# Kernel tuning notes

Measured on AMD Instinct MI355X. Metric: run time of the kernel, lower is better.

## Reference

```python
import jax, jax.numpy as jnp
import numpy as np

N_NODES = 50000
N_EDGES = 800000
D = 128
LN_EPS = 1e-5


def setup_inputs() -> dict:
    key = jax.random.key(0)
    ks = jax.random.split(key, 8)
    s = 1.0 / np.sqrt(D)
    return {
        "x": jax.random.normal(ks[0], (N_NODES, D), jnp.float32),
        "edge_index": jax.random.randint(ks[1], (2, N_EDGES), 0, N_NODES, jnp.int64),
        "W1l": jax.random.normal(ks[2], (D, D), jnp.float32) * s,
        "b1l": jnp.zeros((D,), jnp.float32),
        "W1r": jax.random.normal(ks[3], (D, D), jnp.float32) * s,
        "W2l": jax.random.normal(ks[4], (D, D), jnp.float32) * s,
        "b2l": jnp.zeros((D,), jnp.float32),
        "W2r": jax.random.normal(ks[5], (D, D), jnp.float32) * s,
        "ln_w": jnp.ones((D,), jnp.float32),
        "ln_b": jnp.zeros((D,), jnp.float32),
    }


def _sage_conv(h, edge_index, Wl, bl, Wr):
    # PyG SAGEConv (mean aggr): out = lin_l(mean_{j in N(i)} h_j) + lin_r(h_i)
    src, dst = edge_index[0], edge_index[1]
    n = h.shape[0]
    msg_sum = jax.ops.segment_sum(h[src], dst, num_segments=n)      # [N, D]
    cnt = jax.ops.segment_sum(jnp.ones_like(src, h.dtype), dst, num_segments=n)
    mean = msg_sum / jnp.maximum(cnt, 1.0)[:, None]                  # 0 for isolated
    return mean @ Wl.T + bl + h @ Wr.T


def _layer_norm(h, w, b):
    mu = jnp.mean(h, axis=-1, keepdims=True)
    var = jnp.mean(jnp.square(h - mu), axis=-1, keepdims=True)
    return (h - mu) * jax.lax.rsqrt(var + LN_EPS) * w + b


def reference(x, edge_index, W1l, b1l, W1r, W2l, b2l, W2r, ln_w, ln_b):
    h = jax.nn.relu(_sage_conv(x, edge_index, W1l, b1l, W1r))
    h = jax.nn.relu(_sage_conv(h, edge_index, W2l, b2l, W2r))
    return _layer_norm(h, ln_w, ln_b)
```

## Files before the change

kernel.cpp:

```cpp
#include <hip/hip_runtime.h>

#define DN 128
#define LS 136

typedef short s16x8 __attribute__((ext_vector_type(8)));
typedef float f32x4 __attribute__((ext_vector_type(4)));

__device__ __forceinline__ float bf2f(unsigned short u) {
    union { unsigned int i; float f; } v; v.i = ((unsigned int)u) << 16; return v.f;
}
__device__ __forceinline__ unsigned short f2bf(float f) {
    union { float f; unsigned int i; } v; v.f = f;
    unsigned int r = v.i + 0x7fffu + ((v.i >> 16) & 1u);
    return (unsigned short)(r >> 16);
}
__device__ __forceinline__ float lo16(unsigned int u) { return bf2f((unsigned short)(u & 0xffffu)); }
__device__ __forceinline__ float hi16(unsigned int u) { return bf2f((unsigned short)(u >> 16)); }
__device__ __forceinline__ unsigned int pack2(float x, float y) {
    return (unsigned int)f2bf(x) | ((unsigned int)f2bf(y) << 16);
}
__device__ __forceinline__ float ldx(const void* p, size_t i, int f32) {
    return f32 ? ((const float*)p)[i] : bf2f(((const unsigned short*)p)[i]);
}

__global__ void k_diag(unsigned short* out, int cnt, float val) {
    unsigned short v = f2bf(val);
    for (int i = blockIdx.x * blockDim.x + threadIdx.x; i < cnt; i += gridDim.x * blockDim.x)
        out[i] = v;
}


__global__ __launch_bounds__(1024) void k_packhist(
        const int* e, const void* x,
        const void* W1l, const void* W1r, const void* W2l, const void* W2r,
        const void* b1l, const void* b2l, const void* lnw, const void* lnb,
        int* flags, unsigned int* packed, int* cnt,
        unsigned int* h1, unsigned int* wb, float* biasf, float* lnf,
        int E, int n, int cc) {
    __shared__ int hist[256];
    __shared__ int s_fl[3];
    const int t = threadIdx.x, b = blockIdx.x;
    const int nthr = gridDim.x * 1024;
    const int g = b * 1024 + t;

    if (t < 3) s_fl[t] = 0;
    if (t < 256) hist[t] = 0;
    __syncthreads();
    {
        const unsigned int* xu = (const unsigned int*)x;
        int hit = 0;
#pragma unroll
        for (int i = t; i < 32768; i += 1024) {
            unsigned int u = xu[i];
            if (((u & 0x7F80u) == 0x7F80u) || (((u >> 16) & 0x7F80u) == 0x7F80u)) hit = 1;
        }
        if (hit) atomicOr(&s_fl[0], 1);
        const unsigned int* wu = (const unsigned int*)W1l;
        hit = 0;
#pragma unroll
        for (int i = t; i < 8192; i += 1024) {
            unsigned int u = wu[i];
            if (((u & 0x7F80u) == 0x7F80u) || (((u >> 16) & 0x7F80u) == 0x7F80u)) hit = 1;
        }
        if (hit) atomicOr(&s_fl[2], 1);
        if (t < 1000 && e[2 * t + 1] != 0) atomicOr(&s_fl[1], 1);
    }
    __syncthreads();
    const int xf = s_fl[0], is64 = (s_fl[1] == 0), wf = s_fl[2];
    if (t < 3 && b == 0) { }
    if (t == 0) { flags[0] = s_fl[0]; flags[1] = s_fl[1]; flags[2] = s_fl[2]; }

    const int b0 = b * 4096;
#pragma unroll
    for (int k = 0; k < 4; ++k) {
        int i = b0 + t + k * 1024;
        if (i < E) {
            int d = is64 ? e[2 * (E + i)] : e[E + i];
            int s = is64 ? e[2 * i] : e[i];
            if ((unsigned)s >= (unsigned)n) s = 0;
            unsigned int key = ((unsigned)d < (unsigned)n)
                             ? (((unsigned)d << 16) | (unsigned)s) : 0xFFFF0000u;
            packed[i] = key;
            atomicAdd(&hist[key >> 24], 1);
        }
    }
    if (xf) {
        const float* xp = (const float*)x;
        for (int i = g; i < cc; i += nthr) {
            float2 f = *(const float2*)(xp + 2 * (size_t)i);
            h1[i] = pack2(f.x, f.y);
        }
    } else {
        const unsigned int* xp = (const unsigned int*)x;
        for (int i = g; i < cc; i += nthr) h1[i] = xp[i];
    }
    for (int i = g; i < 32768; i += nthr) {
        int m = i >> 13, el = i & 8191;
        const void* W = (m == 0) ? W1l : (m == 1) ? W1r : (m == 2) ? W2l : W2r;
        unsigned int v;
        if (wf) {
            float2 f = *(const float2*)((const float*)W + 2 * (size_t)el);
            v = pack2(f.x, f.y);
        } else {
            v = ((const unsigned int*)W)[el];
        }
        wb[(size_t)m * 8192 + el] = v;
    }
    if (g < 512) {
        float v;
        if (g < 128)      v = ldx(b1l, g, wf);
        else if (g < 256) v = ldx(b2l, g - 128, wf);
        else if (g < 384) v = ldx(lnw, g - 256, wf);
        else              v = ldx(lnb, g - 384, wf);
        if (g < 256) biasf[g] = v; else lnf[g - 256] = v;
    }
    __syncthreads();
    if (t < 256 && hist[t]) atomicAdd(&cnt[t], hist[t]);
}

__device__ __forceinline__ void scan_cnt(const int* cnt, int* sbase, int t) {
    if (t < 64) {
        int c0 = cnt[4 * t], c1 = cnt[4 * t + 1], c2 = cnt[4 * t + 2], c3 = cnt[4 * t + 3];
        int tot = c0 + c1 + c2 + c3, pre = tot;
#pragma unroll
        for (int off = 1; off < 64; off <<= 1) {
            int u = __shfl_up(pre, off, 64);
            if (t >= off) pre += u;
        }
        int e0 = pre - tot;
        sbase[4 * t] = e0; sbase[4 * t + 1] = e0 + c0;
        sbase[4 * t + 2] = e0 + c0 + c1; sbase[4 * t + 3] = e0 + c0 + c1 + c2;
        if (t == 63) sbase[256] = pre;
    }
}

__global__ __launch_bounds__(1024) void k_p1scat(const unsigned int* in, const int* cnt,
                                                 int* rsv, unsigned int* out, int E) {
    __shared__ int hist[256], lcur[256], gbase[256], sbase[257];
    int t = threadIdx.x;
    int b0 = blockIdx.x * 4096;
    int nb = E - b0; if (nb > 4096) nb = 4096;
    if (t < 256) hist[t] = 0;
    __syncthreads();
    unsigned int v[4];
#pragma unroll
    for (int k = 0; k < 4; ++k) {
        int i = t + k * 1024;
        v[k] = (i < nb) ? in[b0 + i] : 0u;
        if (i < nb) atomicAdd(&hist[v[k] >> 24], 1);
    }
    scan_cnt(cnt, sbase, t);
    __syncthreads();
    if (t < 256) {
        lcur[t] = 0;
        if (hist[t]) gbase[t] = sbase[t] + atomicAdd(&rsv[t], hist[t]);
    }
    __syncthreads();
#pragma unroll
    for (int k = 0; k < 4; ++k) {
        int i = t + k * 1024;
        if (i < nb) {
            unsigned int d = v[k] >> 24;
            int p = atomicAdd(&lcur[d], 1);
            out[gbase[d] + p] = v[k];
        }
    }
}

__global__ __launch_bounds__(1024) void k_p2(const unsigned int* in, const int* cnt,
                                             int* rowp, int* col, int n) {
    __shared__ int hist[256], cur[256], sbase[257];
    int t = threadIdx.x;
    int b = blockIdx.x;
    if (t < 256) hist[t] = 0;
    scan_cnt(cnt, sbase, t);
    __syncthreads();
    int lo = sbase[b], hi = sbase[b + 1];
    if (b == 0 && t == 0) rowp[n] = sbase[196];
    for (int i = lo + t; i < hi; i += 1024)
        atomicAdd(&hist[(in[i] >> 16) & 0xFFu], 1);
    __syncthreads();
    if (t < 64) {
        int h0 = hist[4 * t], h1 = hist[4 * t + 1], h2 = hist[4 * t + 2], h3 = hist[4 * t + 3];
        int tot = h0 + h1 + h2 + h3;
        int pre = tot;
#pragma unroll
        for (int off = 1; off < 64; off <<= 1) {
            int u = __shfl_up(pre, off, 64);
            if (t >= off) pre += u;
        }
        int e0 = pre - tot;
        int e1 = e0 + h0, e2 = e1 + h1, e3 = e2 + h2;
        cur[4 * t] = e0; cur[4 * t + 1] = e1; cur[4 * t + 2] = e2; cur[4 * t + 3] = e3;
        int d0 = b * 256 + 4 * t;
        if (d0 < n)     rowp[d0]     = lo + e0;
        if (d0 + 1 < n) rowp[d0 + 1] = lo + e1;
        if (d0 + 2 < n) rowp[d0 + 2] = lo + e2;
        if (d0 + 3 < n) rowp[d0 + 3] = lo + e3;
    }
    __syncthreads();
    for (int i = lo + t; i < hi; i += 1024) {
        unsigned int v = in[i];
        int p = atomicAdd(&cur[(v >> 16) & 0xFFu], 1);
        col[lo + p] = (int)(v & 0xFFFFu);
    }
}

__global__ void k_gather(const int* rowp, const int* col, const unsigned int* hp,
                         unsigned int* M, int n) {
    int row = blockIdx.x * 4 + (threadIdx.x >> 6);
    if (row >= n) return;
    const int L = threadIdx.x & 63;
    int b = rowp[row], e = rowp[row + 1];
    float s0 = 0.f, s1 = 0.f;
    for (int base = b; base < e; base += 64) {
        int cnt = e - base; if (cnt > 64) cnt = 64;
        int myc = (L < cnt) ? col[base + L] : 0;
        int j = 0;
        for (; j + 8 <= cnt; j += 8) {
            int a0 = __shfl(myc, j + 0, 64);
            int a1 = __shfl(myc, j + 1, 64);
            int a2 = __shfl(myc, j + 2, 64);
            int a3 = __shfl(myc, j + 3, 64);
            int a4 = __shfl(myc, j + 4, 64);
            int a5 = __shfl(myc, j + 5, 64);
            int a6 = __shfl(myc, j + 6, 64);
            int a7 = __shfl(myc, j + 7, 64);
            unsigned int u0 = hp[(size_t)a0 * 64 + L];
            unsigned int u1 = hp[(size_t)a1 * 64 + L];
            unsigned int u2 = hp[(size_t)a2 * 64 + L];
            unsigned int u3 = hp[(size_t)a3 * 64 + L];
            unsigned int u4 = hp[(size_t)a4 * 64 + L];
            unsigned int u5 = hp[(size_t)a5 * 64 + L];
            unsigned int u6 = hp[(size_t)a6 * 64 + L];
            unsigned int u7 = hp[(size_t)a7 * 64 + L];
            s0 += lo16(u0); s1 += hi16(u0);
            s0 += lo16(u1); s1 += hi16(u1);
            s0 += lo16(u2); s1 += hi16(u2);
            s0 += lo16(u3); s1 += hi16(u3);
            s0 += lo16(u4); s1 += hi16(u4);
            s0 += lo16(u5); s1 += hi16(u5);
            s0 += lo16(u6); s1 += hi16(u6);
            s0 += lo16(u7); s1 += hi16(u7);
        }
        for (; j + 4 <= cnt; j += 4) {
            int a0 = __shfl(myc, j + 0, 64);
            int a1 = __shfl(myc, j + 1, 64);
            int a2 = __shfl(myc, j + 2, 64);
            int a3 = __shfl(myc, j + 3, 64);
            unsigned int u0 = hp[(size_t)a0 * 64 + L];
            unsigned int u1 = hp[(size_t)a1 * 64 + L];
            unsigned int u2 = hp[(size_t)a2 * 64 + L];
            unsigned int u3 = hp[(size_t)a3 * 64 + L];
            s0 += lo16(u0); s1 += hi16(u0);
            s0 += lo16(u1); s1 += hi16(u1);
            s0 += lo16(u2); s1 += hi16(u2);
            s0 += lo16(u3); s1 += hi16(u3);
        }
        for (; j < cnt; ++j) {
            int s = __shfl(myc, j, 64);
            unsigned int u = hp[(size_t)s * 64 + L];
            s0 += lo16(u); s1 += hi16(u);
        }
    }
    int d = e - b; if (d < 1) d = 1;
    float inv = 1.0f / (float)d;
    M[(size_t)row * 64 + L] = pack2(s0 * inv, s1 * inv);
}

__global__ __launch_bounds__(512) void k_gemm(
        const unsigned int* M, const unsigned int* hin,
        const unsigned int* wbl, const unsigned int* wbr,
        const float* biasf, const int* flags,
        void* hout, int n, int do_ln, const float* lnwf, const float* lnbf) {
    __shared__ unsigned short sA[128 * LS];
    __shared__ unsigned short sB[128 * LS];
    unsigned int* sAu = (unsigned int*)sA;
    unsigned int* sBu = (unsigned int*)sB;
    const int t = threadIdx.x;
    const int i0 = blockIdx.x * 128;
    const int lane = t & 63, wv = t >> 6, ln15 = lane & 15, quad = lane >> 4;

    f32x4 acc[8];
#pragma unroll
    for (int i = 0; i < 8; ++i) { f32x4 z = {0.f, 0.f, 0.f, 0.f}; acc[i] = z; }

    for (int phase = 0; phase < 2; ++phase) {
        const unsigned int* A = phase ? hin : M;
#pragma unroll
        for (int i = 0; i < 4; ++i) {
            int idx = t + i * 512, r = idx >> 4, c4 = (idx & 15) * 4;
            int node = i0 + r;
            uint4 v = make_uint4(0u, 0u, 0u, 0u);
            if (node < n) v = *(const uint4*)(A + (size_t)node * 64 + c4);
            *(uint4*)(sAu + r * 68 + c4) = v;
        }
        const unsigned int* W = phase ? wbr : wbl;
#pragma unroll
        for (int i = 0; i < 4; ++i) {
            int idx = t + i * 512, r = idx >> 4, c4 = (idx & 15) * 4;
            *(uint4*)(sBu + r * 68 + c4) = *(const uint4*)(W + (size_t)r * 64 + c4);
        }
        __syncthreads();

        const int mrow = wv * 16;
#pragma unroll
        for (int ks = 0; ks < 4; ++ks) {
            s16x8 a = *(const s16x8*)&sA[(mrow + ln15) * LS + ks * 32 + quad * 8];
#pragma unroll
            for (int nt = 0; nt < 8; ++nt) {
                s16x8 bfr = *(const s16x8*)&sB[(nt * 16 + ln15) * LS + ks * 32 + quad * 8];
                acc[nt] = __builtin_amdgcn_mfma_f32_16x16x32_bf16(a, bfr, acc[nt], 0, 0, 0);
            }
        }
        __syncthreads();
    }

#pragma unroll
    for (int nt = 0; nt < 8; ++nt) {
        float bs = biasf[nt * 16 + ln15];
#pragma unroll
        for (int r = 0; r < 4; ++r) {
            float v = acc[nt][r] + bs;
            acc[nt][r] = (v > 0.f) ? v : 0.f;
        }
    }

    if (!do_ln) {
#pragma unroll
        for (int nt = 0; nt < 8; ++nt) {
            int colv = nt * 16 + ln15;
#pragma unroll
            for (int r = 0; r < 4; ++r) {
                int node = i0 + wv * 16 + quad * 4 + r;
                if (node < n)
                    ((unsigned short*)hout)[(size_t)node * DN + colv] = f2bf(acc[nt][r]);
            }
        }
        return;
    }

    const int mix = (flags[0] != flags[2]);
    if (mix) {
#pragma unroll
        for (int nt = 0; nt < 8; ++nt) {
            int colv = nt * 16 + ln15;
#pragma unroll
            for (int r = 0; r < 4; ++r) {
                int node = i0 + wv * 16 + quad * 4 + r;
                if (node < n)
                    ((unsigned short*)hout)[(size_t)node * DN + colv] = 0x442F;
            }
        }
        return;
    }
    const int outf32 = (flags[0] && flags[2]);
    float lw[8], lb[8];
#pragma unroll
    for (int nt = 0; nt < 8; ++nt) {
        lw[nt] = lnwf[nt * 16 + ln15];
        lb[nt] = lnbf[nt * 16 + ln15];
    }
#pragma unroll
    for (int r = 0; r < 4; ++r) {
        float s = 0.f;
#pragma unroll
        for (int nt = 0; nt < 8; ++nt) s += acc[nt][r];
#pragma unroll
        for (int off = 1; off < 16; off <<= 1) s += __shfl_xor(s, off, 64);
        float mu = s * (1.0f / 128.0f);
        float q = 0.f;
#pragma unroll
        for (int nt = 0; nt < 8; ++nt) { float d = acc[nt][r] - mu; q += d * d; }
#pragma unroll
        for (int off = 1; off < 16; off <<= 1) q += __shfl_xor(q, off, 64);
        float rs = rsqrtf(q * (1.0f / 128.0f) + 1e-5f);
        int node = i0 + wv * 16 + quad * 4 + r;
        if (node < n) {
#pragma unroll
            for (int nt = 0; nt < 8; ++nt) {
                int colv = nt * 16 + ln15;
                float o = (acc[nt][r] - mu) * rs * lw[nt] + lb[nt];
                if (outf32) ((float*)hout)[(size_t)node * DN + colv] = o;
                else ((unsigned short*)hout)[(size_t)node * DN + colv] = f2bf(o);
            }
        }
    }
}

extern "C" void kernel_launch(void* const* d_in, const int* in_sizes, int n_in,
                              void* d_out, int out_size, void* d_ws, size_t ws_size,
                              hipStream_t stream) {
    const int N_EXP = 50000, E_EXP = 800000;

    const size_t sz_flags  = 256;
    const size_t sz_rowp   = (((size_t)(N_EXP + 1) * 4) + 255) & ~(size_t)255;
    const size_t sz_cursor = (((size_t)N_EXP * 4) + 255) & ~(size_t)255;
    const size_t sz_col    = (((size_t)E_EXP * 4) + 255) & ~(size_t)255;
    const size_t sz_M      = (size_t)N_EXP * 64 * 4;
    const size_t sz_h      = (size_t)N_EXP * DN * 2;
    const size_t need = sz_flags + sz_rowp + sz_cursor + sz_col + sz_M + sz_h;

    float diag = 0.f;
    if (in_sizes[0] != N_EXP * DN) diag += 1000.f;
    if (in_sizes[1] != 2 * E_EXP)  diag += 2000.f;
    if (n_in != 10)                diag += 4000.f;
    if (out_size != N_EXP * DN)    diag += 8000.f;
    if (ws_size < need)            diag += 16000.f;
    if (diag != 0.f) {
        k_diag<<<1024, 256, 0, stream>>>((unsigned short*)d_out, N_EXP * DN, diag);
        return;
    }

    const void* x   = d_in[0];
    const int*  ei  = (const int*)d_in[1];
    const void* W1l = d_in[2];
    const void* b1l = d_in[3];
    const void* W1r = d_in[4];
    const void* W2l = d_in[5];
    const void* b2l = d_in[6];
    const void* W2r = d_in[7];
    const void* lnw = d_in[8];
    const void* lnb = d_in[9];

    const int n = N_EXP, E = E_EXP;
    int cc = n * 64;

    char* ws = (char*)d_ws;
    int* rowp   = (int*)(ws + sz_flags);
    int* small  = (int*)(ws + sz_flags + sz_rowp);
    int* col    = (int*)(ws + sz_flags + sz_rowp + sz_cursor);
    unsigned int* M  = (unsigned int*)(ws + sz_flags + sz_rowp + sz_cursor + sz_col);
    unsigned int* h1 = (unsigned int*)(ws + sz_flags + sz_rowp + sz_cursor + sz_col + sz_M);

    int* flags = small;
    int* cnt   = small + 64;
    int* rsv   = small + 320;
    unsigned int* wb    = (unsigned int*)(small + 576);
    float* biasf = (float*)(small + 33344);
    float* lnf   = (float*)(small + 33600);
    unsigned int* packed0 = (unsigned int*)col;
    unsigned int* packed1 = (unsigned int*)M;

    hipMemsetAsync(cnt, 0, 2048, stream);

    int P1B = (E + 4095) / 4096;
    k_packhist<<<P1B, 1024, 0, stream>>>(ei, x, W1l, W1r, W2l, W2r,
                                         b1l, b2l, lnw, lnb, flags,
                                         packed0, cnt, h1, wb, biasf, lnf, E, n, cc);
    k_p1scat<<<P1B, 1024, 0, stream>>>(packed0, cnt, rsv, packed1, E);
    k_p2<<<P1B, 1024, 0, stream>>>(packed1, cnt, rowp, col, n);

    int gb = (n + 3) / 4;
    int mb = (n + 127) / 128;

    k_gather<<<gb, 256, 0, stream>>>(rowp, col, h1, M, n);
    k_gemm<<<mb, 512, 0, stream>>>(M, h1, wb, wb + 8192, biasf, flags,
                                   h1, n, 0, nullptr, nullptr);
    k_gather<<<gb, 256, 0, stream>>>(rowp, col, h1, M, n);
    k_gemm<<<mb, 512, 0, stream>>>(M, h1, wb + 16384, wb + 24576, biasf + 128, flags,
                                   d_out, n, 1, lnf, lnf + 128);
}
```

Measured before the change: 211.1 us.

## Fuse CSR scatter passes into one kernel with per-block histograms and grid barrier

Each block of the first pass now writes its own 256-bin histogram into a matrix instead of adding into a global counter. The fused kernel derives its bucket base offsets by scanning that matrix directly, so the global reservation atomics and the memset of the counters are no longer needed. The two scatter passes (high-byte bucket, then per-row) are merged into one launch, separated by a spin-wait grid barrier on a done counter that the previous kernel resets. This removes a kernel launch and a memset. In exchange, every block redundantly reads the whole 196x256 histogram matrix, and correctness now depends on all 196 blocks being co-resident on the GPU.

New measurement: 232.7 us. 10.3% more time.

```diff
diff --git a/kernel.cpp b/kernel.cpp
--- a/kernel.cpp
+++ b/kernel.cpp
@@ -34,7 +34,7 @@
         const int* e, const void* x,
         const void* W1l, const void* W1r, const void* W2l, const void* W2r,
         const void* b1l, const void* b2l, const void* lnw, const void* lnb,
-        int* flags, unsigned int* packed, int* cnt,
+        int* flags, unsigned int* packed, int* histmat,
         unsigned int* h1, unsigned int* wb, float* biasf, float* lnf,
         int E, int n, int cc) {
     __shared__ int hist[256];
@@ -67,8 +67,10 @@
     }
     __syncthreads();
     const int xf = s_fl[0], is64 = (s_fl[1] == 0), wf = s_fl[2];
-    if (t < 3 && b == 0) { }
-    if (t == 0) { flags[0] = s_fl[0]; flags[1] = s_fl[1]; flags[2] = s_fl[2]; }
+    if (t == 0) {
+        flags[0] = s_fl[0]; flags[1] = s_fl[1]; flags[2] = s_fl[2];
+        flags[8] = 0;
+    }
 
     const int b0 = b * 4096;
 #pragma unroll
@@ -115,70 +117,71 @@
         if (g < 256) biasf[g] = v; else lnf[g - 256] = v;
     }
     __syncthreads();
-    if (t < 256 && hist[t]) atomicAdd(&cnt[t], hist[t]);
-}
-
-__device__ __forceinline__ void scan_cnt(const int* cnt, int* sbase, int t) {
+    if (t < 256) histmat[b * 256 + t] = hist[t];
+}
+
+__global__ __launch_bounds__(1024) void k_p12(
+        const unsigned int* in, const int* histmat,
+        unsigned int* scat, int* rowp, int* col, int* done, int E, int n) {
+    __shared__ int hist[256], lcur[256], gbase[256], cur[256], sbase[257];
+    const int t = threadIdx.x, b = blockIdx.x;
+
+    if (t < 256) {
+        int tot = 0, pre = 0;
+        for (int bp = 0; bp < 196; ++bp) {
+            int h = histmat[bp * 256 + t];
+            tot += h;
+            if (bp < b) pre += h;
+        }
+        hist[t] = tot;
+        lcur[t] = pre;
+    }
+    __syncthreads();
     if (t < 64) {
-        int c0 = cnt[4 * t], c1 = cnt[4 * t + 1], c2 = cnt[4 * t + 2], c3 = cnt[4 * t + 3];
-        int tot = c0 + c1 + c2 + c3, pre = tot;
+        int c0 = hist[4 * t], c1 = hist[4 * t + 1], c2 = hist[4 * t + 2], c3 = hist[4 * t + 3];
+        int tot4 = c0 + c1 + c2 + c3, pre = tot4;
 #pragma unroll
         for (int off = 1; off < 64; off <<= 1) {
             int u = __shfl_up(pre, off, 64);
             if (t >= off) pre += u;
         }
-        int e0 = pre - tot;
+        int e0 = pre - tot4;
         sbase[4 * t] = e0; sbase[4 * t + 1] = e0 + c0;
         sbase[4 * t + 2] = e0 + c0 + c1; sbase[4 * t + 3] = e0 + c0 + c1 + c2;
         if (t == 63) sbase[256] = pre;
     }
-}
-
-__global__ __launch_bounds__(1024) void k_p1scat(const unsigned int* in, const int* cnt,
-                                                 int* rsv, unsigned int* out, int E) {
-    __shared__ int hist[256], lcur[256], gbase[256], sbase[257];
-    int t = threadIdx.x;
-    int b0 = blockIdx.x * 4096;
-    int nb = E - b0; if (nb > 4096) nb = 4096;
-    if (t < 256) hist[t] = 0;
-    __syncthreads();
-    unsigned int v[4];
+    __syncthreads();
+    if (t < 256) {
+        gbase[t] = sbase[t] + lcur[t];
+        lcur[t] = 0;
+    }
+    __syncthreads();
+    const int b0 = b * 4096;
 #pragma unroll
     for (int k = 0; k < 4; ++k) {
-        int i = t + k * 1024;
-        v[k] = (i < nb) ? in[b0 + i] : 0u;
-        if (i < nb) atomicAdd(&hist[v[k] >> 24], 1);
-    }
-    scan_cnt(cnt, sbase, t);
-    __syncthreads();
-    if (t < 256) {
-        lcur[t] = 0;
-        if (hist[t]) gbase[t] = sbase[t] + atomicAdd(&rsv[t], hist[t]);
-    }
-    __syncthreads();
-#pragma unroll
-    for (int k = 0; k < 4; ++k) {
-        int i = t + k * 1024;
-        if (i < nb) {
-            unsigned int d = v[k] >> 24;
+        int i = b0 + t + k * 1024;
+        if (i < E) {
+            unsigned int v = in[i];
+            unsigned int d = v >> 24;
             int p = atomicAdd(&lcur[d], 1);
-            out[gbase[d] + p] = v[k];
-        }
-    }
-}
-
-__global__ __launch_bounds__(1024) void k_p2(const unsigned int* in, const int* cnt,
-                                             int* rowp, int* col, int n) {
-    __shared__ int hist[256], cur[256], sbase[257];
-    int t = threadIdx.x;
-    int b = blockIdx.x;
-    if (t < 256) hist[t] = 0;
-    scan_cnt(cnt, sbase, t);
-    __syncthreads();
+            scat[gbase[d] + p] = v;
+        }
+    }
+    __syncthreads();
+    if (t == 0) {
+        __threadfence();
+        atomicAdd(done, 1);
+        while (atomicAdd(done, 0) < 196) __builtin_amdgcn_s_sleep(8);
+        __threadfence();
+    }
+    __syncthreads();
+
     int lo = sbase[b], hi = sbase[b + 1];
     if (b == 0 && t == 0) rowp[n] = sbase[196];
+    if (t < 256) hist[t] = 0;
+    __syncthreads();
     for (int i = lo + t; i < hi; i += 1024)
-        atomicAdd(&hist[(in[i] >> 16) & 0xFFu], 1);
+        atomicAdd(&hist[(scat[i] >> 16) & 0xFFu], 1);
     __syncthreads();
     if (t < 64) {
         int h0 = hist[4 * t], h1 = hist[4 * t + 1], h2 = hist[4 * t + 2], h3 = hist[4 * t + 3];
@@ -200,7 +203,7 @@
     }
     __syncthreads();
     for (int i = lo + t; i < hi; i += 1024) {
-        unsigned int v = in[i];
+        unsigned int v = scat[i];
         int p = atomicAdd(&cur[(v >> 16) & 0xFFu], 1);
         col[lo + p] = (int)(v & 0xFFFFu);
     }
@@ -434,22 +437,18 @@
     unsigned int* h1 = (unsigned int*)(ws + sz_flags + sz_rowp + sz_cursor + sz_col + sz_M);
 
     int* flags = small;
-    int* cnt   = small + 64;
-    int* rsv   = small + 320;
     unsigned int* wb    = (unsigned int*)(small + 576);
     float* biasf = (float*)(small + 33344);
     float* lnf   = (float*)(small + 33600);
     unsigned int* packed0 = (unsigned int*)col;
-    unsigned int* packed1 = (unsigned int*)M;
-
-    hipMemsetAsync(cnt, 0, 2048, stream);
+    unsigned int* scat    = (unsigned int*)M;
+    int* histmat          = (int*)(M + E_EXP);
 
     int P1B = (E + 4095) / 4096;
     k_packhist<<<P1B, 1024, 0, stream>>>(ei, x, W1l, W1r, W2l, W2r,
                                          b1l, b2l, lnw, lnb, flags,
-                                         packed0, cnt, h1, wb, biasf, lnf, E, n, cc);
-    k_p1scat<<<P1B, 1024, 0, stream>>>(packed0, cnt, rsv, packed1, E);
-    k_p2<<<P1B, 1024, 0, stream>>>(packed1, cnt, rowp, col, n);
+                                         packed0, histmat, h1, wb, biasf, lnf, E, n, cc);
+    k_p12<<<P1B, 1024, 0, stream>>>(packed0, histmat, scat, rowp, col, &flags[8], E, n);
 
     int gb = (n + 3) / 4;
     int mb = (n + 127) / 128;
```
